# Optimization experiments

Measured on AMD Instinct MI355X. Metric: run time of the kernel, lower is better.

The kernel has to match this reference:

```python
import jax, jax.numpy as jnp
import numpy as np

B, N, F_IN, T = 2, 10000, 32, 16
E = 160000
K = 3
C_CHEB = 64
C_TIME = 64
STRIDE = 1
LN_EPS = 1e-5


def setup_inputs() -> dict:
    key = jax.random.key(0)
    ks = jax.random.split(key, 8)
    x = jax.random.normal(ks[0], (B, N, F_IN, T), dtype=jnp.float32)
    edge_index = jax.random.randint(ks[1], (2, E), 0, N, dtype=jnp.int32)
    cheb_W = jax.random.normal(ks[2], (K, F_IN, C_CHEB), dtype=jnp.float32) / np.float32(np.sqrt(F_IN))
    cheb_b = jnp.zeros((C_CHEB,), jnp.float32)
    time_W = jax.random.normal(ks[3], (C_TIME, C_CHEB, 1, 3), dtype=jnp.float32) / np.float32(np.sqrt(C_CHEB * 3))
    time_b = jnp.zeros((C_TIME,), jnp.float32)
    res_W = jax.random.normal(ks[4], (C_TIME, F_IN, 1, 1), dtype=jnp.float32) / np.float32(np.sqrt(F_IN))
    res_b = jnp.zeros((C_TIME,), jnp.float32)
    ln_g = jnp.ones((C_TIME,), jnp.float32)
    ln_b = jnp.zeros((C_TIME,), jnp.float32)
    return dict(x=x, edge_index=edge_index, cheb_W=cheb_W, cheb_b=cheb_b,
                time_W=time_W, time_b=time_b, res_W=res_W, res_b=res_b,
                ln_g=ln_g, ln_b=ln_b)


def _mstgcn_block(x, edge_index, cheb_W, cheb_b, time_W, time_b, res_W, res_b, ln_g, ln_b):
    row, col = edge_index[0], edge_index[1]
    # PyG ChebConv with normalization='sym', lambda_max=2: L_hat = -D^{-1/2} A D^{-1/2}
    deg = jax.ops.segment_sum(jnp.ones((E,), x.dtype), row, num_segments=N)
    dinv = jnp.where(deg > 0, jax.lax.rsqrt(jnp.where(deg > 0, deg, 1.0)), 0.0)
    w = -(dinv[row] * dinv[col])  # (E,)

    def prop(z):  # z: (B,N,F,T) -> L_hat @ z along node axis, all timesteps batched
        zn = jnp.moveaxis(z, 1, 0)                      # (N,B,F,T)
        msg = zn[row] * w[:, None, None, None]          # (E,B,F,T)
        agg = jax.ops.segment_sum(msg, col, num_segments=N)
        return jnp.moveaxis(agg, 0, 1)                  # (B,N,F,T)

    # Chebyshev recursion: Tx0=x, Tx1=L_hat x, Tx_k = 2 L_hat Tx_{k-1} - Tx_{k-2}
    Tx0 = x
    out = jnp.einsum('bnft,fo->bnot', Tx0, cheb_W[0])
    Tx1 = prop(x)
    out = out + jnp.einsum('bnft,fo->bnot', Tx1, cheb_W[1])
    for k in range(2, K):
        Tx2 = 2.0 * prop(Tx1) - Tx0
        out = out + jnp.einsum('bnft,fo->bnot', Tx2, cheb_W[k])
        Tx0, Tx1 = Tx1, Tx2
    out = out + cheb_b[None, None, :, None]

    spatial_gcn = jax.nn.relu(out)                      # (B,N,C_cheb,T)
    spc = jnp.transpose(spatial_gcn, (0, 2, 1, 3))      # (B,C_cheb,N,T)
    tc = jax.lax.conv_general_dilated(
        spc, time_W, window_strides=(1, STRIDE), padding=((0, 0), (1, 1)),
        dimension_numbers=('NCHW', 'OIHW', 'NCHW')) + time_b[None, :, None, None]

    xc = jnp.transpose(x, (0, 2, 1, 3))                 # (B,F_in,N,T)
    res = jax.lax.conv_general_dilated(
        xc, res_W, window_strides=(1, STRIDE), padding=((0, 0), (0, 0)),
        dimension_numbers=('NCHW', 'OIHW', 'NCHW')) + res_b[None, :, None, None]

    z = jax.nn.relu(res + tc)                           # (B,C_time,N,T_out)
    zp = jnp.transpose(z, (0, 3, 2, 1))                 # (B,T_out,N,C_time)
    mu = jnp.mean(zp, axis=-1, keepdims=True)
    var = jnp.mean((zp - mu) ** 2, axis=-1, keepdims=True)
    ln = (zp - mu) * jax.lax.rsqrt(var + LN_EPS) * ln_g + ln_b
    return jnp.transpose(ln, (0, 2, 3, 1))              # (B,N,C_time,T_out)


def reference(x, edge_index, cheb_W, cheb_b, time_W, time_b, res_W, res_b, ln_g, ln_b):
    return _mstgcn_block(x, edge_index, cheb_W, cheb_b, time_W, time_b, res_W, res_b, ln_g, ln_b)
```

## Files before the change

kernel.cpp:

```cpp
#include <hip/hip_runtime.h>


#define F_IN 32
#define TT   16
#define CCH  64
#define FTN  512
#define WPB  4
#define WSTR 1600

__global__ void k_edge1(const int* __restrict__ row, const int* __restrict__ col,
                        float* __restrict__ deg, int* __restrict__ cnt,
                        int* __restrict__ pos, int E) {
    int i = blockIdx.x * 256 + threadIdx.x;
    if (i < E) {
        atomicAdd(&deg[row[i]], 1.0f);
        pos[i] = atomicAdd(&cnt[col[i]], 1);
    }
}

__global__ void k_scan(const int* __restrict__ cnt, int* __restrict__ rowptr, int n) {
    __shared__ int sdata[1024];
    int tid = threadIdx.x;
    int run = 0;
    for (int base = 0; base < n; base += 1024) {
        int v = (base + tid < n) ? cnt[base + tid] : 0;
        sdata[tid] = v;
        __syncthreads();
        for (int off = 1; off < 1024; off <<= 1) {
            int add = (tid >= off) ? sdata[tid - off] : 0;
            __syncthreads();
            sdata[tid] += add;
            __syncthreads();
        }
        int incl  = sdata[tid];
        int total = sdata[1023];
        if (base + tid < n) rowptr[base + tid] = run + incl - v;
        run += total;
        __syncthreads();
    }
    if (tid == 0) rowptr[n] = run;
}

__global__ void k_fill(const int* __restrict__ row, const int* __restrict__ col,
                       const float* __restrict__ deg, const int* __restrict__ rowptr,
                       const int* __restrict__ pos, int* __restrict__ srcs,
                       float* __restrict__ wsort, int E) {
    int i = blockIdx.x * 256 + threadIdx.x;
    if (i < E) {
        int r = row[i], c = col[i];
        float dr = deg[r], dc = deg[c];
        float w = 0.0f;
        if (dr > 0.0f && dc > 0.0f) w = -(rsqrtf(dr) * rsqrtf(dc));
        int slot = rowptr[c] + pos[i];
        srcs[slot]  = r;
        wsort[slot] = w;
    }
}

__global__ void k_prop(const float* __restrict__ zin, float* __restrict__ zout,
                       const int* __restrict__ rowptr, const int* __restrict__ srcs,
                       const float* __restrict__ wsort, int N) {
    int n   = blockIdx.x;
    int tid = threadIdx.x;
    int beg = rowptr[n], end = rowptr[n + 1];
    const size_t bstride = (size_t)N * FTN;
    const size_t eoff = (size_t)(tid >> 7) * bstride + (size_t)(tid & 127) * 4;

    float4 a = make_float4(0.f, 0.f, 0.f, 0.f);
    int j = beg;
    for (; j + 3 < end; j += 4) {
        int   s0 = srcs[j],  s1 = srcs[j + 1], s2 = srcs[j + 2], s3 = srcs[j + 3];
        float w0 = wsort[j], w1 = wsort[j + 1], w2 = wsort[j + 2], w3 = wsort[j + 3];
        float4 v0 = *reinterpret_cast<const float4*>(zin + (size_t)s0 * FTN + eoff);
        float4 v1 = *reinterpret_cast<const float4*>(zin + (size_t)s1 * FTN + eoff);
        float4 v2 = *reinterpret_cast<const float4*>(zin + (size_t)s2 * FTN + eoff);
        float4 v3 = *reinterpret_cast<const float4*>(zin + (size_t)s3 * FTN + eoff);
        a.x = fmaf(w0, v0.x, fmaf(w1, v1.x, fmaf(w2, v2.x, fmaf(w3, v3.x, a.x))));
        a.y = fmaf(w0, v0.y, fmaf(w1, v1.y, fmaf(w2, v2.y, fmaf(w3, v3.y, a.y))));
        a.z = fmaf(w0, v0.z, fmaf(w1, v1.z, fmaf(w2, v2.z, fmaf(w3, v3.z, a.z))));
        a.w = fmaf(w0, v0.w, fmaf(w1, v1.w, fmaf(w2, v2.w, fmaf(w3, v3.w, a.w))));
    }
    for (; j < end; ++j) {
        int   s0 = srcs[j];
        float w0 = wsort[j];
        float4 v0 = *reinterpret_cast<const float4*>(zin + (size_t)s0 * FTN + eoff);
        a.x = fmaf(w0, v0.x, a.x);
        a.y = fmaf(w0, v0.y, a.y);
        a.z = fmaf(w0, v0.z, a.z);
        a.w = fmaf(w0, v0.w, a.w);
    }
    *reinterpret_cast<float4*>(zout + (size_t)n * FTN + eoff) = a;
}

__global__ void k_prep(const float* __restrict__ cheb_W, const float* __restrict__ time_W,
                       const float* __restrict__ res_W,
                       float* __restrict__ Wabc, float* __restrict__ tWt, float* __restrict__ rWt) {
    int i = blockIdx.x * 256 + threadIdx.x;
    if (i < F_IN * 64) {
        int f = i >> 6, o = i & 63;
        float w0 = cheb_W[(0 * F_IN + f) * 64 + o];
        float w1 = cheb_W[(1 * F_IN + f) * 64 + o];
        float w2 = cheb_W[(2 * F_IN + f) * 64 + o];
        Wabc[i]          = w0 - w2;
        Wabc[2048 + i]   = w1;
        Wabc[4096 + i]   = 2.0f * w2;
        rWt[i] = res_W[o * F_IN + f];
    }
    if (i < 64 * 3 * 64) {
        int ci = i / 192, r = i % 192, dt = r >> 6, co = r & 63;
        tWt[i] = time_W[(co * 64 + ci) * 3 + dt];
    }
}

__global__ __launch_bounds__(256) void k_fused(
        const float* __restrict__ x, const float* __restrict__ P1, const float* __restrict__ P2,
        const float* __restrict__ Wabc, const float* __restrict__ rWt, const float* __restrict__ tWt,
        const float* __restrict__ cheb_b, const float* __restrict__ time_b,
        const float* __restrict__ res_b, const float* __restrict__ ln_g,
        const float* __restrict__ ln_b, float* __restrict__ out, int N) {
    __shared__ float smem[WPB * WSTR];
    int lane = threadIdx.x & 63;
    int wib  = threadIdx.x >> 6;
    int co   = lane;
    float chb = cheb_b[co], tb = time_b[co], rb = res_b[co];
    float lng = ln_g[co],   lnb = ln_b[co];
    float*  st = smem + wib * WSTR;
    float4* s4 = reinterpret_cast<float4*>(st);

    int gw = blockIdx.x * WPB + wib;
    int nw = gridDim.x * WPB;
    int nitems = 2 * N;
    const size_t bstride = (size_t)N * FTN;

    for (int item = gw; item < nitems; item += nw) {
        int b = (item >= N) ? 1 : 0;
        int n = item - b * N;
        const float4* x4 = reinterpret_cast<const float4*>(x  + b * bstride + (size_t)n * FTN);
        const float4* a4 = reinterpret_cast<const float4*>(P1 + b * bstride + (size_t)n * FTN);
        const float4* b4 = reinterpret_cast<const float4*>(P2 + b * bstride + (size_t)n * FTN);

        float4 xv0 = x4[lane], xv1 = x4[64 + lane];
        float4 av0 = a4[lane], av1 = a4[64 + lane];
        float4 bv0 = b4[lane], bv1 = b4[64 + lane];
        s4[lane]       = xv0;  s4[64 + lane]  = xv1;
        s4[128 + lane] = av0;  s4[192 + lane] = av1;
        s4[256 + lane] = bv0;  s4[320 + lane] = bv1;

        float acc[16], res[16];
#pragma unroll
        for (int t = 0; t < 16; ++t) { acc[t] = chb; res[t] = rb; }

        for (int f = 0; f < F_IN; ++f) {
            float wa = Wabc[f * 64 + co];
            float wb = Wabc[2048 + f * 64 + co];
            float wc = Wabc[4096 + f * 64 + co];
            float wr = rWt[f * 64 + co];
#pragma unroll
            for (int q = 0; q < 4; ++q) {
                float4 xv = s4[f * 4 + q];
                float4 av = s4[128 + f * 4 + q];
                float4 bv = s4[256 + f * 4 + q];
                acc[q*4+0] = fmaf(wa, xv.x, fmaf(wb, av.x, fmaf(wc, bv.x, acc[q*4+0])));
                acc[q*4+1] = fmaf(wa, xv.y, fmaf(wb, av.y, fmaf(wc, bv.y, acc[q*4+1])));
                acc[q*4+2] = fmaf(wa, xv.z, fmaf(wb, av.z, fmaf(wc, bv.z, acc[q*4+2])));
                acc[q*4+3] = fmaf(wa, xv.w, fmaf(wb, av.w, fmaf(wc, bv.w, acc[q*4+3])));
                res[q*4+0] = fmaf(wr, xv.x, res[q*4+0]);
                res[q*4+1] = fmaf(wr, xv.y, res[q*4+1]);
                res[q*4+2] = fmaf(wr, xv.z, res[q*4+2]);
                res[q*4+3] = fmaf(wr, xv.w, res[q*4+3]);
            }
        }

        st[co * 20 + 0] = 0.f; st[co * 20 + 17] = 0.f;
        st[co * 20 + 18] = 0.f; st[co * 20 + 19] = 0.f;
#pragma unroll
        for (int t = 0; t < 16; ++t) st[co * 20 + t + 1] = fmaxf(acc[t], 0.f);

#pragma unroll
        for (int t = 0; t < 16; ++t) acc[t] = res[t] + tb;
        for (int ci = 0; ci < 64; ++ci) {
            float w0 = tWt[ci * 192 + co];
            float w1 = tWt[ci * 192 + 64 + co];
            float w2 = tWt[ci * 192 + 128 + co];
            const float4* srow = reinterpret_cast<const float4*>(st + ci * 20);
            float4 s0 = srow[0], s1 = srow[1], s2 = srow[2], s3 = srow[3], s4v = srow[4];
            float s[20] = { s0.x,s0.y,s0.z,s0.w, s1.x,s1.y,s1.z,s1.w,
                            s2.x,s2.y,s2.z,s2.w, s3.x,s3.y,s3.z,s3.w,
                            s4v.x,s4v.y,s4v.z,s4v.w };
#pragma unroll
            for (int t = 0; t < 16; ++t)
                acc[t] = fmaf(w0, s[t], fmaf(w1, s[t + 1], fmaf(w2, s[t + 2], acc[t])));
        }

        float z[16];
#pragma unroll
        for (int t = 0; t < 16; ++t) {
            float zz = fmaxf(acc[t], 0.f);
            float p1 = zz, p2 = zz * zz;
#pragma unroll
            for (int off = 32; off >= 1; off >>= 1) {
                p1 += __shfl_xor(p1, off);
                p2 += __shfl_xor(p2, off);
            }
            float mu  = p1 * (1.0f / 64.0f);
            float var = p2 * (1.0f / 64.0f) - mu * mu;
            z[t] = (zz - mu) * rsqrtf(var + 1e-5f) * lng + lnb;
        }
        float4* o4 = reinterpret_cast<float4*>(out + (size_t)item * 1024 + co * 16);
        o4[0] = make_float4(z[0],  z[1],  z[2],  z[3]);
        o4[1] = make_float4(z[4],  z[5],  z[6],  z[7]);
        o4[2] = make_float4(z[8],  z[9],  z[10], z[11]);
        o4[3] = make_float4(z[12], z[13], z[14], z[15]);
    }
}

extern "C" void kernel_launch(void* const* d_in, const int* in_sizes, int n_in,
                              void* d_out, int out_size, void* d_ws, size_t ws_size,
                              hipStream_t stream) {
    const float* x      = (const float*)d_in[0];
    const int*   ei     = (const int*)d_in[1];
    const float* cheb_W = (const float*)d_in[2];
    const float* cheb_b = (const float*)d_in[3];
    const float* time_W = (const float*)d_in[4];
    const float* time_b = (const float*)d_in[5];
    const float* res_W  = (const float*)d_in[6];
    const float* res_b  = (const float*)d_in[7];
    const float* ln_g   = (const float*)d_in[8];
    const float* ln_b   = (const float*)d_in[9];
    float* out = (float*)d_out;

    const int N = in_sizes[0] / (2 * F_IN * TT);
    const int E = in_sizes[1] / 2;
    const int* row = ei;
    const int* col = ei + E;

    char* w = (char*)d_ws;
    size_t off = 0;
    auto carve = [&](size_t bytes) { off = (off + 255) & ~(size_t)255; size_t o = off; off += bytes; return o; };
    float* deg    = (float*)(w + carve((size_t)N * 4));
    int*   cnt    = (int*)  (w + carve((size_t)N * 4));
    int*   rowptr = (int*)  (w + carve((size_t)(N + 1) * 4));
    int*   pos    = (int*)  (w + carve((size_t)E * 4));
    int*   srcs   = (int*)  (w + carve((size_t)E * 4));
    float* wsort  = (float*)(w + carve((size_t)E * 4));
    float* Wabc   = (float*)(w + carve(3 * 32 * 64 * 4));
    float* tWt    = (float*)(w + carve(64 * 3 * 64 * 4));
    float* rWt    = (float*)(w + carve(32 * 64 * 4));
    float* P1     = (float*)(w + carve((size_t)2 * N * FTN * 4));
    float* P2     = (float*)(w + carve((size_t)2 * N * FTN * 4));
    (void)ws_size; (void)n_in; (void)out_size;

    hipMemsetAsync(deg, 0, (size_t)N * 4, stream);
    hipMemsetAsync(cnt, 0, (size_t)N * 4, stream);

    int eb = (E + 255) / 256;
    k_edge1<<<eb, 256, 0, stream>>>(row, col, deg, cnt, pos, E);
    k_scan<<<1, 1024, 0, stream>>>(cnt, rowptr, N);
    k_fill<<<eb, 256, 0, stream>>>(row, col, deg, rowptr, pos, srcs, wsort, E);
    k_prop<<<N, 256, 0, stream>>>(x,  P1, rowptr, srcs, wsort, N);
    k_prop<<<N, 256, 0, stream>>>(P1, P2, rowptr, srcs, wsort, N);
    k_prep<<<48, 256, 0, stream>>>(cheb_W, time_W, res_W, Wabc, tWt, rWt);

    int items  = 2 * N;
    int blocks = (items + WPB - 1) / WPB;
    k_fused<<<blocks, 64 * WPB, 0, stream>>>(x, P1, P2, Wabc, rWt, tWt,
                                             cheb_b, time_b, res_b, ln_g, ln_b, out, N);
}
```

Before: 585.2 us.

## Use split-bf16 MFMA for Chebyshev, residual and temporal conv matmuls

Replaces the scalar FMA loops of the fused epilogue kernel with 16x16x32 bf16 MFMA instructions. Each fp32 operand is split into a high and a low bf16 part, and three MFMAs are accumulated to keep accuracy close to fp32. Weights are prepacked into MFMA fragment layout by a new prep kernel. The temporal conv is done as three time-shifted matmuls whose results are combined with lane shuffles. The intent is to cut ALU time in the fused kernel, at the cost of extra conversion work and a small loss of precision.

Result: faster. 477.2 us (-18.5%).

```diff
diff --git a/kernel.cpp b/kernel.cpp
--- a/kernel.cpp
+++ b/kernel.cpp
@@ -3,10 +3,21 @@
 
 #define F_IN 32
 #define TT   16
-#define CCH  64
 #define FTN  512
 #define WPB  4
-#define WSTR 1600
+
+typedef __attribute__((ext_vector_type(8))) short bf16x8;
+typedef __attribute__((ext_vector_type(4))) float f32x4;
+#define MFMA __builtin_amdgcn_mfma_f32_16x16x32_bf16
+
+__device__ __forceinline__ unsigned short f2bf(float v) {
+    unsigned int u = __float_as_uint(v);
+    unsigned int r = (u + 0x7FFFu + ((u >> 16) & 1u)) >> 16;
+    return (unsigned short)r;
+}
+__device__ __forceinline__ float bf2f(unsigned short h) {
+    return __uint_as_float(((unsigned int)h) << 16);
+}
 
 __global__ void k_edge1(const int* __restrict__ row, const int* __restrict__ col,
                         float* __restrict__ deg, int* __restrict__ cnt,
@@ -92,40 +103,85 @@
     *reinterpret_cast<float4*>(zout + (size_t)n * FTN + eoff) = a;
 }
 
-__global__ void k_prep(const float* __restrict__ cheb_W, const float* __restrict__ time_W,
-                       const float* __restrict__ res_W,
-                       float* __restrict__ Wabc, float* __restrict__ tWt, float* __restrict__ rWt) {
-    int i = blockIdx.x * 256 + threadIdx.x;
-    if (i < F_IN * 64) {
-        int f = i >> 6, o = i & 63;
-        float w0 = cheb_W[(0 * F_IN + f) * 64 + o];
-        float w1 = cheb_W[(1 * F_IN + f) * 64 + o];
-        float w2 = cheb_W[(2 * F_IN + f) * 64 + o];
-        Wabc[i]          = w0 - w2;
-        Wabc[2048 + i]   = w1;
-        Wabc[4096 + i]   = 2.0f * w2;
-        rWt[i] = res_W[o * F_IN + f];
-    }
-    if (i < 64 * 3 * 64) {
-        int ci = i / 192, r = i % 192, dt = r >> 6, co = r & 63;
-        tWt[i] = time_W[(co * 64 + ci) * 3 + dt];
+__device__ __forceinline__ uint4 pack_frag(const float* w, int h) {
+    unsigned short s[8];
+#pragma unroll
+    for (int j = 0; j < 8; ++j) {
+        float v = w[j];
+        unsigned short hi = f2bf(v);
+        s[j] = h ? f2bf(v - bf2f(hi)) : hi;
+    }
+    uint4 u;
+    u.x = (unsigned)s[0] | ((unsigned)s[1] << 16);
+    u.y = (unsigned)s[2] | ((unsigned)s[3] << 16);
+    u.z = (unsigned)s[4] | ((unsigned)s[5] << 16);
+    u.w = (unsigned)s[6] | ((unsigned)s[7] << 16);
+    return u;
+}
+
+__global__ void k_prepf(const float* __restrict__ cheb_W, const float* __restrict__ time_W,
+                        const float* __restrict__ res_W,
+                        uint4* __restrict__ pBa, uint4* __restrict__ pBr,
+                        uint4* __restrict__ pBt) {
+    int tid = blockIdx.x * 256 + threadIdx.x;
+    if (tid >= 5120) return;
+    int lane = tid & 63, g = lane >> 4, mm = lane & 15;
+    float w[8];
+    if (tid < 1536) {
+        int fa = tid >> 6;
+        int h = fa & 1, nt = (fa >> 1) & 3, ks = fa >> 3;
+        int co = nt * 16 + mm;
+#pragma unroll
+        for (int j = 0; j < 8; ++j) {
+            int f = g * 8 + j;
+            float v;
+            if (ks == 0)      v = cheb_W[f * 64 + co] - cheb_W[4096 + f * 64 + co];
+            else if (ks == 1) v = cheb_W[2048 + f * 64 + co];
+            else              v = 2.0f * cheb_W[4096 + f * 64 + co];
+            w[j] = v;
+        }
+        pBa[fa * 64 + lane] = pack_frag(w, h);
+    } else if (tid < 2048) {
+        int fr = (tid - 1536) >> 6;
+        int h = fr & 1, nt = fr >> 1;
+        int co = nt * 16 + mm;
+#pragma unroll
+        for (int j = 0; j < 8; ++j) w[j] = res_W[co * 32 + (g * 8 + j)];
+        pBr[fr * 64 + lane] = pack_frag(w, h);
+    } else {
+        int ft = (tid - 2048) >> 6;
+        int h = ft & 1, nt = (ft >> 1) & 3, ks = (ft >> 3) & 1, dt = ft >> 4;
+        int co = nt * 16 + mm;
+#pragma unroll
+        for (int j = 0; j < 8; ++j) {
+            int ci = ks * 32 + g * 8 + j;
+            w[j] = time_W[(co * 64 + ci) * 3 + dt];
+        }
+        pBt[ft * 64 + lane] = pack_frag(w, h);
     }
 }
 
 __global__ __launch_bounds__(256) void k_fused(
         const float* __restrict__ x, const float* __restrict__ P1, const float* __restrict__ P2,
-        const float* __restrict__ Wabc, const float* __restrict__ rWt, const float* __restrict__ tWt,
+        const uint4* __restrict__ pBa, const uint4* __restrict__ pBr,
+        const uint4* __restrict__ pBt,
         const float* __restrict__ cheb_b, const float* __restrict__ time_b,
         const float* __restrict__ res_b, const float* __restrict__ ln_g,
         const float* __restrict__ ln_b, float* __restrict__ out, int N) {
-    __shared__ float smem[WPB * WSTR];
+    __shared__ float sgAll[WPB][16][68];
     int lane = threadIdx.x & 63;
     int wib  = threadIdx.x >> 6;
-    int co   = lane;
-    float chb = cheb_b[co], tb = time_b[co], rb = res_b[co];
-    float lng = ln_g[co],   lnb = ln_b[co];
-    float*  st = smem + wib * WSTR;
-    float4* s4 = reinterpret_cast<float4*>(st);
+    int g    = lane >> 4;
+    int mm   = lane & 15;
+    float (*sgT)[68] = sgAll[wib];
+
+    float chb[4], tbb[4], rbb[4], lng[4], lnb[4];
+#pragma unroll
+    for (int nt = 0; nt < 4; ++nt) {
+        int co = nt * 16 + mm;
+        chb[nt] = cheb_b[co]; tbb[nt] = time_b[co]; rbb[nt] = res_b[co];
+        lng[nt] = ln_g[co];   lnb[nt] = ln_b[co];
+    }
 
     int gw = blockIdx.x * WPB + wib;
     int nw = gridDim.x * WPB;
@@ -135,82 +191,155 @@
     for (int item = gw; item < nitems; item += nw) {
         int b = (item >= N) ? 1 : 0;
         int n = item - b * N;
-        const float4* x4 = reinterpret_cast<const float4*>(x  + b * bstride + (size_t)n * FTN);
-        const float4* a4 = reinterpret_cast<const float4*>(P1 + b * bstride + (size_t)n * FTN);
-        const float4* b4 = reinterpret_cast<const float4*>(P2 + b * bstride + (size_t)n * FTN);
-
-        float4 xv0 = x4[lane], xv1 = x4[64 + lane];
-        float4 av0 = a4[lane], av1 = a4[64 + lane];
-        float4 bv0 = b4[lane], bv1 = b4[64 + lane];
-        s4[lane]       = xv0;  s4[64 + lane]  = xv1;
-        s4[128 + lane] = av0;  s4[192 + lane] = av1;
-        s4[256 + lane] = bv0;  s4[320 + lane] = bv1;
-
-        float acc[16], res[16];
-#pragma unroll
-        for (int t = 0; t < 16; ++t) { acc[t] = chb; res[t] = rb; }
-
-        for (int f = 0; f < F_IN; ++f) {
-            float wa = Wabc[f * 64 + co];
-            float wb = Wabc[2048 + f * 64 + co];
-            float wc = Wabc[4096 + f * 64 + co];
-            float wr = rWt[f * 64 + co];
-#pragma unroll
-            for (int q = 0; q < 4; ++q) {
-                float4 xv = s4[f * 4 + q];
-                float4 av = s4[128 + f * 4 + q];
-                float4 bv = s4[256 + f * 4 + q];
-                acc[q*4+0] = fmaf(wa, xv.x, fmaf(wb, av.x, fmaf(wc, bv.x, acc[q*4+0])));
-                acc[q*4+1] = fmaf(wa, xv.y, fmaf(wb, av.y, fmaf(wc, bv.y, acc[q*4+1])));
-                acc[q*4+2] = fmaf(wa, xv.z, fmaf(wb, av.z, fmaf(wc, bv.z, acc[q*4+2])));
-                acc[q*4+3] = fmaf(wa, xv.w, fmaf(wb, av.w, fmaf(wc, bv.w, acc[q*4+3])));
-                res[q*4+0] = fmaf(wr, xv.x, res[q*4+0]);
-                res[q*4+1] = fmaf(wr, xv.y, res[q*4+1]);
-                res[q*4+2] = fmaf(wr, xv.z, res[q*4+2]);
-                res[q*4+3] = fmaf(wr, xv.w, res[q*4+3]);
-            }
-        }
-
-        st[co * 20 + 0] = 0.f; st[co * 20 + 17] = 0.f;
-        st[co * 20 + 18] = 0.f; st[co * 20 + 19] = 0.f;
-#pragma unroll
-        for (int t = 0; t < 16; ++t) st[co * 20 + t + 1] = fmaxf(acc[t], 0.f);
-
-#pragma unroll
-        for (int t = 0; t < 16; ++t) acc[t] = res[t] + tb;
-        for (int ci = 0; ci < 64; ++ci) {
-            float w0 = tWt[ci * 192 + co];
-            float w1 = tWt[ci * 192 + 64 + co];
-            float w2 = tWt[ci * 192 + 128 + co];
-            const float4* srow = reinterpret_cast<const float4*>(st + ci * 20);
-            float4 s0 = srow[0], s1 = srow[1], s2 = srow[2], s3 = srow[3], s4v = srow[4];
-            float s[20] = { s0.x,s0.y,s0.z,s0.w, s1.x,s1.y,s1.z,s1.w,
-                            s2.x,s2.y,s2.z,s2.w, s3.x,s3.y,s3.z,s3.w,
-                            s4v.x,s4v.y,s4v.z,s4v.w };
-#pragma unroll
-            for (int t = 0; t < 16; ++t)
-                acc[t] = fmaf(w0, s[t], fmaf(w1, s[t + 1], fmaf(w2, s[t + 2], acc[t])));
-        }
-
-        float z[16];
-#pragma unroll
-        for (int t = 0; t < 16; ++t) {
-            float zz = fmaxf(acc[t], 0.f);
-            float p1 = zz, p2 = zz * zz;
-#pragma unroll
-            for (int off = 32; off >= 1; off >>= 1) {
-                p1 += __shfl_xor(p1, off);
-                p2 += __shfl_xor(p2, off);
-            }
-            float mu  = p1 * (1.0f / 64.0f);
-            float var = p2 * (1.0f / 64.0f) - mu * mu;
-            z[t] = (zz - mu) * rsqrtf(var + 1e-5f) * lng + lnb;
-        }
-        float4* o4 = reinterpret_cast<float4*>(out + (size_t)item * 1024 + co * 16);
-        o4[0] = make_float4(z[0],  z[1],  z[2],  z[3]);
-        o4[1] = make_float4(z[4],  z[5],  z[6],  z[7]);
-        o4[2] = make_float4(z[8],  z[9],  z[10], z[11]);
-        o4[3] = make_float4(z[12], z[13], z[14], z[15]);
+        const float* bx  = x  + b * bstride + (size_t)n * FTN;
+        const float* bp1 = P1 + b * bstride + (size_t)n * FTN;
+        const float* bp2 = P2 + b * bstride + (size_t)n * FTN;
+
+        float a1[3][8];
+#pragma unroll
+        for (int j = 0; j < 8; ++j) {
+            int off = (g * 8 + j) * 16 + mm;
+            a1[0][j] = bx[off];
+            a1[1][j] = bp1[off];
+            a1[2][j] = bp2[off];
+        }
+        bf16x8 a1h[3], a1l[3];
+#pragma unroll
+        for (int ks = 0; ks < 3; ++ks)
+#pragma unroll
+            for (int j = 0; j < 8; ++j) {
+                float v = a1[ks][j];
+                unsigned short hi = f2bf(v);
+                a1h[ks][j] = (short)hi;
+                a1l[ks][j] = (short)f2bf(v - bf2f(hi));
+            }
+
+        f32x4 acc[4], res[4];
+#pragma unroll
+        for (int nt = 0; nt < 4; ++nt) { acc[nt] = (f32x4){0,0,0,0}; res[nt] = (f32x4){0,0,0,0}; }
+#pragma unroll
+        for (int ks = 0; ks < 3; ++ks)
+#pragma unroll
+            for (int nt = 0; nt < 4; ++nt) {
+                bf16x8 bh = *reinterpret_cast<const bf16x8*>(&pBa[((ks*4+nt)*2 + 0)*64 + lane]);
+                bf16x8 bl = *reinterpret_cast<const bf16x8*>(&pBa[((ks*4+nt)*2 + 1)*64 + lane]);
+                acc[nt] = MFMA(a1h[ks], bh, acc[nt], 0, 0, 0);
+                acc[nt] = MFMA(a1l[ks], bh, acc[nt], 0, 0, 0);
+                acc[nt] = MFMA(a1h[ks], bl, acc[nt], 0, 0, 0);
+            }
+#pragma unroll
+        for (int nt = 0; nt < 4; ++nt) {
+            bf16x8 bh = *reinterpret_cast<const bf16x8*>(&pBr[(nt*2 + 0)*64 + lane]);
+            bf16x8 bl = *reinterpret_cast<const bf16x8*>(&pBr[(nt*2 + 1)*64 + lane]);
+            res[nt] = MFMA(a1h[0], bh, res[nt], 0, 0, 0);
+            res[nt] = MFMA(a1l[0], bh, res[nt], 0, 0, 0);
+            res[nt] = MFMA(a1h[0], bl, res[nt], 0, 0, 0);
+        }
+
+#pragma unroll
+        for (int nt = 0; nt < 4; ++nt) {
+            int co = nt * 16 + mm;
+            sgT[g*4 + 0][co] = fmaxf(acc[nt].x + chb[nt], 0.f);
+            sgT[g*4 + 1][co] = fmaxf(acc[nt].y + chb[nt], 0.f);
+            sgT[g*4 + 2][co] = fmaxf(acc[nt].z + chb[nt], 0.f);
+            sgT[g*4 + 3][co] = fmaxf(acc[nt].w + chb[nt], 0.f);
+        }
+
+        bf16x8 a2h[2], a2l[2];
+#pragma unroll
+        for (int ks = 0; ks < 2; ++ks) {
+            const float* rp = &sgT[mm][ks*32 + g*8];
+            float4 v0 = *reinterpret_cast<const float4*>(rp);
+            float4 v1 = *reinterpret_cast<const float4*>(rp + 4);
+            float vv[8] = {v0.x, v0.y, v0.z, v0.w, v1.x, v1.y, v1.z, v1.w};
+#pragma unroll
+            for (int j = 0; j < 8; ++j) {
+                unsigned short hi = f2bf(vv[j]);
+                a2h[ks][j] = (short)hi;
+                a2l[ks][j] = (short)f2bf(vv[j] - bf2f(hi));
+            }
+        }
+
+        f32x4 oA[4];
+#pragma unroll
+        for (int nt = 0; nt < 4; ++nt) {
+            oA[nt].x = res[nt].x + rbb[nt] + tbb[nt];
+            oA[nt].y = res[nt].y + rbb[nt] + tbb[nt];
+            oA[nt].z = res[nt].z + rbb[nt] + tbb[nt];
+            oA[nt].w = res[nt].w + rbb[nt] + tbb[nt];
+        }
+
+#pragma unroll
+        for (int dt = 0; dt < 3; ++dt) {
+            f32x4 D[4];
+#pragma unroll
+            for (int nt = 0; nt < 4; ++nt) D[nt] = (f32x4){0,0,0,0};
+#pragma unroll
+            for (int ks = 0; ks < 2; ++ks)
+#pragma unroll
+                for (int nt = 0; nt < 4; ++nt) {
+                    int ft = ((dt*2 + ks)*4 + nt)*2;
+                    bf16x8 bh = *reinterpret_cast<const bf16x8*>(&pBt[(ft + 0)*64 + lane]);
+                    bf16x8 bl = *reinterpret_cast<const bf16x8*>(&pBt[(ft + 1)*64 + lane]);
+                    D[nt] = MFMA(a2h[ks], bh, D[nt], 0, 0, 0);
+                    D[nt] = MFMA(a2l[ks], bh, D[nt], 0, 0, 0);
+                    D[nt] = MFMA(a2h[ks], bl, D[nt], 0, 0, 0);
+                }
+            if (dt == 1) {
+#pragma unroll
+                for (int nt = 0; nt < 4; ++nt) {
+                    oA[nt].x += D[nt].x; oA[nt].y += D[nt].y;
+                    oA[nt].z += D[nt].z; oA[nt].w += D[nt].w;
+                }
+            } else if (dt == 0) {
+#pragma unroll
+                for (int nt = 0; nt < 4; ++nt) {
+                    float up = __shfl(D[nt].w, lane - 16);
+                    oA[nt].x += (g == 0) ? 0.f : up;
+                    oA[nt].y += D[nt].x; oA[nt].z += D[nt].y; oA[nt].w += D[nt].z;
+                }
+            } else {
+#pragma unroll
+                for (int nt = 0; nt < 4; ++nt) {
+                    float dn = __shfl(D[nt].x, lane + 16);
+                    oA[nt].x += D[nt].y; oA[nt].y += D[nt].z; oA[nt].z += D[nt].w;
+                    oA[nt].w += (g == 3) ? 0.f : dn;
+                }
+            }
+        }
+
+        float s1[4] = {0,0,0,0}, s2[4] = {0,0,0,0};
+#pragma unroll
+        for (int nt = 0; nt < 4; ++nt) {
+            oA[nt].x = fmaxf(oA[nt].x, 0.f); s1[0] += oA[nt].x; s2[0] = fmaf(oA[nt].x, oA[nt].x, s2[0]);
+            oA[nt].y = fmaxf(oA[nt].y, 0.f); s1[1] += oA[nt].y; s2[1] = fmaf(oA[nt].y, oA[nt].y, s2[1]);
+            oA[nt].z = fmaxf(oA[nt].z, 0.f); s1[2] += oA[nt].z; s2[2] = fmaf(oA[nt].z, oA[nt].z, s2[2]);
+            oA[nt].w = fmaxf(oA[nt].w, 0.f); s1[3] += oA[nt].w; s2[3] = fmaf(oA[nt].w, oA[nt].w, s2[3]);
+        }
+#pragma unroll
+        for (int off = 1; off <= 8; off <<= 1)
+#pragma unroll
+            for (int r = 0; r < 4; ++r) {
+                s1[r] += __shfl_xor(s1[r], off);
+                s2[r] += __shfl_xor(s2[r], off);
+            }
+        float mu[4], ri[4];
+#pragma unroll
+        for (int r = 0; r < 4; ++r) {
+            mu[r] = s1[r] * (1.0f / 64.0f);
+            float var = s2[r] * (1.0f / 64.0f) - mu[r] * mu[r];
+            ri[r] = rsqrtf(var + 1e-5f);
+        }
+        float* ob = out + (size_t)item * 1024;
+#pragma unroll
+        for (int nt = 0; nt < 4; ++nt) {
+            float4 o;
+            o.x = (oA[nt].x - mu[0]) * ri[0] * lng[nt] + lnb[nt];
+            o.y = (oA[nt].y - mu[1]) * ri[1] * lng[nt] + lnb[nt];
+            o.z = (oA[nt].z - mu[2]) * ri[2] * lng[nt] + lnb[nt];
+            o.w = (oA[nt].w - mu[3]) * ri[3] * lng[nt] + lnb[nt];
+            *reinterpret_cast<float4*>(ob + (nt*16 + mm)*16 + g*4) = o;
+        }
     }
 }
 
@@ -243,9 +372,9 @@
     int*   pos    = (int*)  (w + carve((size_t)E * 4));
     int*   srcs   = (int*)  (w + carve((size_t)E * 4));
     float* wsort  = (float*)(w + carve((size_t)E * 4));
-    float* Wabc   = (float*)(w + carve(3 * 32 * 64 * 4));
-    float* tWt    = (float*)(w + carve(64 * 3 * 64 * 4));
-    float* rWt    = (float*)(w + carve(32 * 64 * 4));
+    uint4* pBa    = (uint4*)(w + carve((size_t)24 * 64 * 16));
+    uint4* pBr    = (uint4*)(w + carve((size_t)8  * 64 * 16));
+    uint4* pBt    = (uint4*)(w + carve((size_t)48 * 64 * 16));
     float* P1     = (float*)(w + carve((size_t)2 * N * FTN * 4));
     float* P2     = (float*)(w + carve((size_t)2 * N * FTN * 4));
     (void)ws_size; (void)n_in; (void)out_size;
@@ -259,10 +388,10 @@
     k_fill<<<eb, 256, 0, stream>>>(row, col, deg, rowptr, pos, srcs, wsort, E);
     k_prop<<<N, 256, 0, stream>>>(x,  P1, rowptr, srcs, wsort, N);
     k_prop<<<N, 256, 0, stream>>>(P1, P2, rowptr, srcs, wsort, N);
-    k_prep<<<48, 256, 0, stream>>>(cheb_W, time_W, res_W, Wabc, tWt, rWt);
+    k_prepf<<<20, 256, 0, stream>>>(cheb_W, time_W, res_W, pBa, pBr, pBt);
 
     int items  = 2 * N;
     int blocks = (items + WPB - 1) / WPB;
-    k_fused<<<blocks, 64 * WPB, 0, stream>>>(x, P1, P2, Wabc, rWt, tWt,
+    k_fused<<<blocks, 64 * WPB, 0, stream>>>(x, P1, P2, pBa, pBr, pBt,
                                              cheb_b, time_b, res_b, ln_g, ln_b, out, N);
 }
```
